# Kernel tuning notes

Measured on AMD Instinct MI355X. Metric: run time of the kernel, lower is better.

## Reference

```python
import jax, jax.numpy as jnp
import numpy as np

L, H, N = 4096, 256, 64  # seq_len, hidden_size, hippo_n
EPS = 1e-5


def setup_inputs() -> dict:
    key = jax.random.key(0)
    ks = jax.random.split(key, 8)
    x = jax.random.normal(ks[0], (L, H), jnp.float32)
    # S4D-Lin style initialization for the diagonal SSM (H independent SSMs of state size N)
    Lambda_re = -0.5 * jnp.ones((H, N), jnp.float32)
    Lambda_im = jnp.tile(jnp.pi * jnp.arange(N, dtype=jnp.float32), (H, 1))
    B_re = jnp.ones((H, N), jnp.float32)
    B_im = jnp.zeros((H, N), jnp.float32)
    C_re = jax.random.normal(ks[1], (H, N), jnp.float32) * (0.5 ** 0.5)
    C_im = jax.random.normal(ks[2], (H, N), jnp.float32) * (0.5 ** 0.5)
    D = jax.random.normal(ks[3], (H,), jnp.float32)
    log_step = jax.random.uniform(ks[4], (H,), jnp.float32,
                                  minval=jnp.log(0.001), maxval=jnp.log(0.1))
    ln_w = jnp.ones((H,), jnp.float32)
    ln_b = jnp.zeros((H,), jnp.float32)
    sc = 1.0 / jnp.sqrt(jnp.float32(H))
    W1 = jax.random.normal(ks[5], (H, H), jnp.float32) * sc
    b1 = jnp.zeros((H,), jnp.float32)
    W2 = jax.random.normal(ks[6], (H, H), jnp.float32) * sc
    b2 = jnp.zeros((H,), jnp.float32)
    return {"x": x, "Lambda_re": Lambda_re, "Lambda_im": Lambda_im,
            "B_re": B_re, "B_im": B_im, "C_re": C_re, "C_im": C_im,
            "D": D, "log_step": log_step, "ln_w": ln_w, "ln_b": ln_b,
            "W1": W1, "b1": b1, "W2": W2, "b2": b2}


def reference(x, Lambda_re, Lambda_im, B_re, B_im, C_re, C_im, D, log_step,
              ln_w, ln_b, W1, b1, W2, b2):
    skip = x
    # per-token LayerNorm over the H feature axis (eqx.nn.LayerNorm, eps=1e-5)
    mu = jnp.mean(x, axis=-1, keepdims=True)
    var = jnp.mean(jnp.square(x - mu), axis=-1, keepdims=True)
    xn = (x - mu) / jnp.sqrt(var + EPS) * ln_w + ln_b  # [L, H]

    # ZOH discretization of the diagonal SSM (the cell.ssm(L) step)
    Lam = Lambda_re + 1j * Lambda_im                     # [H, N] complex64
    dt = jnp.exp(log_step)[:, None]                      # [H, 1]
    Ab = jnp.exp(Lam * dt)                               # [H, N]
    Bb = (Ab - 1.0) / Lam * (B_re + 1j * B_im)           # [H, N]
    C = C_re + 1j * C_im                                 # [H, N]

    def step(s, u):  # s: [H, N] complex state, u: [H] input at one time step
        s = Ab * s + Bb * u[:, None]
        y = 2.0 * jnp.einsum('hn,hn->h', C, s).real + D * u
        return s, y

    s0 = jnp.zeros((H, N), jnp.complex64)
    hidden, ys = jax.lax.scan(step, s0, xn)              # ys: [L, H]

    g = jax.nn.gelu(ys)
    out = (g @ W1.T + b1) * jax.nn.sigmoid(g @ W2.T + b2)  # GLU epilogue
    return (hidden, skip + out)
```

## Files before the change

kernel.cpp:

```cpp
#include <hip/hip_runtime.h>
#include <hip/hip_bf16.h>

#define LSEQ 4096
#define HDIM 256
#define NS   64
#define PC   32
#define MC   128

typedef __attribute__((ext_vector_type(8))) short short8;
typedef __attribute__((ext_vector_type(4))) float floatx4;

__device__ __forceinline__ short b16(float x) {
    __hip_bfloat16 h = __float2bfloat16(x);
    return *(reinterpret_cast<short*>(&h));
}
__device__ __forceinline__ unsigned int pk2(float a, float b) {
    return (unsigned int)(unsigned short)b16(a) | ((unsigned int)(unsigned short)b16(b) << 16);
}
__device__ __forceinline__ void cmul(float& xr, float& xi, float yr, float yi) {
    float r = xr * yr - xi * yi;
    float i = xr * yi + xi * yr;
    xr = r; xi = i;
}

__global__ __launch_bounds__(256) void k_pre(const float* __restrict__ x,
                                             const float* __restrict__ lnw,
                                             const float* __restrict__ lnb,
                                             const float* __restrict__ W1,
                                             const float* __restrict__ W2,
                                             float* __restrict__ xnT,
                                             unsigned short* __restrict__ w1b,
                                             unsigned short* __restrict__ w2b) {
    int t = threadIdx.x;
    if (blockIdx.x >= 256) {
        int g = (blockIdx.x - 256) * 256 + t;
        float4 a = ((const float4*)W1)[g];
        float4 c = ((const float4*)W2)[g];
        ushort4 o1, o2;
        o1.x = (unsigned short)b16(a.x); o1.y = (unsigned short)b16(a.y);
        o1.z = (unsigned short)b16(a.z); o1.w = (unsigned short)b16(a.w);
        o2.x = (unsigned short)b16(c.x); o2.y = (unsigned short)b16(c.y);
        o2.z = (unsigned short)b16(c.z); o2.w = (unsigned short)b16(c.w);
        ((ushort4*)w1b)[g] = o1;
        ((ushort4*)w2b)[g] = o2;
        return;
    }
    __shared__ float tile[16][257];
    __shared__ float smu[16], srs[16];
    int l0 = blockIdx.x * 16;
#pragma unroll
    for (int i = 0; i < 16; ++i)
        tile[i][t] = x[(size_t)(l0 + i) * HDIM + t];
    __syncthreads();
    int wv = t >> 6, lane = t & 63;
#pragma unroll
    for (int k = 0; k < 4; ++k) {
        int i = wv * 4 + k;
        float s = 0.f, s2 = 0.f;
#pragma unroll
        for (int q = 0; q < 4; ++q) {
            float v = tile[i][lane + 64 * q];
            s += v; s2 += v * v;
        }
#pragma unroll
        for (int o = 32; o; o >>= 1) {
            s  += __shfl_xor(s, o);
            s2 += __shfl_xor(s2, o);
        }
        if (lane == 0) {
            float m = s * (1.0f / HDIM);
            smu[i] = m;
            srs[i] = rsqrtf(s2 * (1.0f / HDIM) - m * m + 1e-5f);
        }
    }
    __syncthreads();
    float wh = lnw[t], bh = lnb[t];
    float o[16];
#pragma unroll
    for (int i = 0; i < 16; ++i)
        o[i] = (tile[i][t] - smu[i]) * srs[i] * wh + bh;
    float4* dst = (float4*)(xnT + (size_t)t * LSEQ + l0);
#pragma unroll
    for (int k = 0; k < 4; ++k)
        dst[k] = make_float4(o[4 * k], o[4 * k + 1], o[4 * k + 2], o[4 * k + 3]);
}

__device__ __forceinline__ void ssm_consts(const float* Lre, const float* Lim,
                                           const float* Bre, const float* Bim,
                                           float dt, int idx,
                                           float& are, float& aim, float& bre, float& bim) {
    float lre = Lre[idx], lim = Lim[idx];
    float er = expf(lre * dt);
    float sa, ca;
    sincosf(lim * dt, &sa, &ca);
    are = er * ca; aim = er * sa;
    float inv = 1.0f / (lre * lre + lim * lim);
    float nre = are - 1.0f, nim = aim;
    float tre = (nre * lre + nim * lim) * inv;
    float tim = (nim * lre - nre * lim) * inv;
    float br = Bre[idx], bi = Bim[idx];
    bre = tre * br - tim * bi;
    bim = tre * bi + tim * br;
}

__global__ __launch_bounds__(256) void k_scan(const float* __restrict__ xnT,
                                              const float* __restrict__ Lre,
                                              const float* __restrict__ Lim,
                                              const float* __restrict__ Bre,
                                              const float* __restrict__ Bim,
                                              const float* __restrict__ Cre,
                                              const float* __restrict__ Cim,
                                              const float* __restrict__ Dv,
                                              const float* __restrict__ lstep,
                                              __hip_bfloat16* __restrict__ gb,
                                              float* __restrict__ hid,
                                              int interleaved) {
    __shared__ __align__(16) unsigned char ldsb[60672];
    short* ubf = (short*)(ldsb);
    short* Tm  = (short*)(ldsb + 8704);
    float* Ff  = (float*)(ldsb + 43520);
    short* S0s = (short*)(ldsb + 43520);
    float* Kt  = (float*)(ldsb + 60160);

    int h = blockIdx.x;
    int tid = threadIdx.x;
    int wv = __builtin_amdgcn_readfirstlane(tid) >> 6;
    int lane = tid & 63;
    int l15 = lane & 15, q = lane >> 4;
    const float* uh = xnT + (size_t)h * LSEQ;

    float dt = expf(lstep[h]);
    float Dh = Dv[h];

    float are, aim, bre, bim;
    ssm_consts(Lre, Lim, Bre, Bim, dt, h * NS + lane, are, aim, bre, bim);
    float cre = Cre[h * NS + lane], cim = Cim[h * NS + lane];

    float A8r = are, A8i = aim;
    cmul(A8r, A8i, A8r, A8i); cmul(A8r, A8i, A8r, A8i); cmul(A8r, A8i, A8r, A8i);
    float A16r = A8r, A16i = A8i;  cmul(A16r, A16i, A16r, A16i);
    float A32r = A16r, A32i = A16i; cmul(A32r, A32i, A32r, A32i);
    float A64r = A32r, A64i = A32i; cmul(A64r, A64i, A64r, A64i);

#pragma unroll
    for (int k = 0; k < 4; ++k) {
        int i4 = k * 1024 + tid * 4;
        float4 v = *(const float4*)(uh + i4);
        int c = i4 >> 7, col = i4 & 127;
        unsigned int* d = (unsigned int*)(ubf + c * 136 + col);
        d[0] = pk2(v.x, v.y);
        d[1] = pk2(v.z, v.w);
    }

    {
        float cbre = cre * bre - cim * bim;
        float cbim = cre * bim + cim * bre;
        float pr = 1.f, pi = 0.f;
        if (wv & 1) cmul(pr, pi, A32r, A32i);
        if (wv & 2) cmul(pr, pi, A64r, A64i);
        for (int i = 0; i < 32; ++i) {
            float kj = 2.f * (cbre * pr - cbim * pi);
#pragma unroll
            for (int o = 1; o <= 32; o <<= 1) kj += __shfl_xor(kj, o);
            if (lane == 0) Kt[32 * wv + i] = kj;
            cmul(pr, pi, are, aim);
        }
    }
    __syncthreads();

#pragma unroll 4
    for (int it = 0; it < 64; ++it) {
        int idx = it * 256 + tid;
        int row = idx >> 7, col = idx & 127;
        float kv = Kt[(row - col) & 127];
        Tm[row * 136 + col] = (col <= row) ? b16(kv) : (short)0;
    }

    {
        int n2 = 16 * wv + l15;
        float are2, aim2, bre2, bim2;
        ssm_consts(Lre, Lim, Bre, Bim, dt, h * NS + n2, are2, aim2, bre2, bim2);
        float B8r = are2, B8i = aim2;
        cmul(B8r, B8i, B8r, B8i); cmul(B8r, B8i, B8r, B8i); cmul(B8r, B8i, B8r, B8i);
        float B16r = B8r, B16i = B8i;  cmul(B16r, B16i, B16r, B16i);
        float B32r = B16r, B32i = B16i; cmul(B32r, B32i, B32r, B32i);
        float B64r = B32r, B64i = B32i; cmul(B64r, B64i, B64r, B64i);

        floatx4 fR[2], fI[2];
#pragma unroll
        for (int nt = 0; nt < 2; ++nt) { fR[nt] = (floatx4){0,0,0,0}; fI[nt] = (floatx4){0,0,0,0}; }

#pragma unroll
        for (int ks = 0; ks < 4; ++ks) {
            int m8 = 15 - 4 * ks - q;
            float sR = 1.f, sI = 0.f, tR, tI;
            tR = sR * B8r - sI * B8i;  tI = sR * B8i + sI * B8r;
            sR = (m8 & 1) ? tR : sR;   sI = (m8 & 1) ? tI : sI;
            tR = sR * B16r - sI * B16i; tI = sR * B16i + sI * B16r;
            sR = (m8 & 2) ? tR : sR;   sI = (m8 & 2) ? tI : sI;
            tR = sR * B32r - sI * B32i; tI = sR * B32i + sI * B32r;
            sR = (m8 & 4) ? tR : sR;   sI = (m8 & 4) ? tI : sI;
            tR = sR * B64r - sI * B64i; tI = sR * B64i + sI * B64r;
            sR = (m8 & 8) ? tR : sR;   sI = (m8 & 8) ? tI : sI;
            short8 aR, aI;
            float curR = sR, curI = sI;
#pragma unroll
            for (int e = 7; e >= 0; --e) {
                aR[e] = b16(bre2 * curR - bim2 * curI);
                aI[e] = b16(bre2 * curI + bim2 * curR);
                if (e) cmul(curR, curI, are2, aim2);
            }
#pragma unroll
            for (int nt = 0; nt < 2; ++nt) {
                short8 bf = *(short8*)(ubf + (16 * nt + l15) * 136 + 32 * ks + 8 * q);
                fR[nt] = __builtin_amdgcn_mfma_f32_16x16x32_bf16(aR, bf, fR[nt], 0, 0, 0);
                fI[nt] = __builtin_amdgcn_mfma_f32_16x16x32_bf16(aI, bf, fI[nt], 0, 0, 0);
            }
        }
#pragma unroll
        for (int nt = 0; nt < 2; ++nt) {
            int c = 16 * nt + l15;
            float* fp = Ff + c * 130;
#pragma unroll
            for (int reg = 0; reg < 4; ++reg) {
                int ns = 16 * wv + q * 4 + reg;
                fp[ns]      = fR[nt][reg];
                fp[65 + ns] = fI[nt][reg];
            }
        }
    }
    __syncthreads();

    if (wv == 0) {
        float a128r = A64r, a128i = A64i;
        cmul(a128r, a128i, A64r, A64i);
        float sre = 0.f, sim = 0.f;
        for (int c = 0; c < PC; ++c) {
            float fre = Ff[c * 130 + lane];
            float fim = Ff[c * 130 + 65 + lane];
            ((unsigned int*)(ldsb + 43520 + 272 * c))[lane] = pk2(sre, sim);
            float nr = fmaf(a128r, sre, fmaf(-a128i, sim, fre));
            float ni = fmaf(a128r, sim, fmaf( a128i, sre, fim));
            sre = nr; sim = ni;
        }
        if (interleaved) {
            ((float2*)hid)[h * NS + lane] = make_float2(sre, sim);
        } else {
            hid[h * NS + lane] = sre;
        }
    }

    floatx4 Y[2][2];
#pragma unroll
    for (int mi = 0; mi < 2; ++mi)
#pragma unroll
        for (int nt = 0; nt < 2; ++nt) Y[mi][nt] = (floatx4){0, 0, 0, 0};

#pragma unroll
    for (int ks = 0; ks < 4; ++ks) {
        short8 bf0 = *(short8*)(ubf + l15 * 136 + 32 * ks + 8 * q);
        short8 bf1 = *(short8*)(ubf + (16 + l15) * 136 + 32 * ks + 8 * q);
#pragma unroll
        for (int mi = 0; mi < 2; ++mi) {
            int row = 16 * (2 * wv + mi) + l15;
            short8 ta = *(short8*)(Tm + row * 136 + 32 * ks + 8 * q);
            Y[mi][0] = __builtin_amdgcn_mfma_f32_16x16x32_bf16(ta, bf0, Y[mi][0], 0, 0, 0);
            Y[mi][1] = __builtin_amdgcn_mfma_f32_16x16x32_bf16(ta, bf1, Y[mi][1], 0, 0, 0);
        }
    }
    __syncthreads();

    {
        float pr = 1.f, pi = 0.f;
        if (wv & 1) cmul(pr, pi, A32r, A32i);
        if (wv & 2) cmul(pr, pi, A64r, A64i);
        cmul(pr, pi, are, aim);
        for (int i = 0; i < 32; ++i) {
            int t = 32 * wv + i;
            float er =  2.f * (cre * pr - cim * pi);
            float en = -2.f * (cre * pi + cim * pr);
            ((unsigned int*)(ldsb + 8704 + 272 * t))[lane] = pk2(er, en);
            cmul(pr, pi, are, aim);
        }
    }
    __syncthreads();

#pragma unroll
    for (int ks = 0; ks < 4; ++ks) {
        short8 sf0 = *(short8*)(S0s + l15 * 136 + 32 * ks + 8 * q);
        short8 sf1 = *(short8*)(S0s + (16 + l15) * 136 + 32 * ks + 8 * q);
#pragma unroll
        for (int mi = 0; mi < 2; ++mi) {
            int row = 16 * (2 * wv + mi) + l15;
            short8 ea = *(short8*)(Tm + row * 136 + 32 * ks + 8 * q);
            Y[mi][0] = __builtin_amdgcn_mfma_f32_16x16x32_bf16(ea, sf0, Y[mi][0], 0, 0, 0);
            Y[mi][1] = __builtin_amdgcn_mfma_f32_16x16x32_bf16(ea, sf1, Y[mi][1], 0, 0, 0);
        }
    }

#pragma unroll
    for (int mi = 0; mi < 2; ++mi) {
#pragma unroll
        for (int nt = 0; nt < 2; ++nt) {
#pragma unroll
            for (int reg = 0; reg < 4; ++reg) {
                int t = 16 * (2 * wv + mi) + q * 4 + reg;
                int c = 16 * nt + l15;
                int l = c * MC + t;
                float u = uh[l];
                float y = Y[mi][nt][reg] + Dh * u;
                float z = 0.7978845608028654f * fmaf(0.044715f, y * y * y, y);
                float e = __expf(2.f * z);
                float th = 1.f - 2.f / (e + 1.f);
                float gg = 0.5f * y * (1.f + th);
                gb[((size_t)l << 8) + h] = __float2bfloat16(gg);
            }
        }
    }
}

__global__ __launch_bounds__(64) void k_glu_mfma(const unsigned short* __restrict__ gbs,
                                                 const unsigned short* __restrict__ w1b,
                                                 const unsigned short* __restrict__ w2b,
                                                 const float* __restrict__ b1v,
                                                 const float* __restrict__ b2v,
                                                 const float* __restrict__ x,
                                                 float* __restrict__ out) {
    int bx = blockIdx.x;
    int m0 = (bx >> 3) * 32;
    int n0 = (bx & 7) * 32;
    int lane = threadIdx.x;
    int t = lane & 15, q = lane >> 4;

    floatx4 acc[2][2][2];
#pragma unroll
    for (int a = 0; a < 2; ++a)
#pragma unroll
        for (int b = 0; b < 2; ++b)
#pragma unroll
            for (int g = 0; g < 2; ++g)
                acc[a][b][g] = (floatx4){0.f, 0.f, 0.f, 0.f};

    const unsigned short* A0  = gbs + (size_t)(m0 + t) * HDIM + q * 8;
    const unsigned short* A1  = A0 + 16 * HDIM;
    const unsigned short* B10 = w1b + (size_t)(n0 + t) * HDIM + q * 8;
    const unsigned short* B11 = B10 + 16 * HDIM;
    const unsigned short* B20 = w2b + (size_t)(n0 + t) * HDIM + q * 8;
    const unsigned short* B21 = B20 + 16 * HDIM;

#pragma unroll
    for (int ks = 0; ks < 8; ++ks) {
        int off = ks * 32;
        short8 a0  = *(const short8*)(A0  + off);
        short8 a1  = *(const short8*)(A1  + off);
        short8 b10 = *(const short8*)(B10 + off);
        short8 b11 = *(const short8*)(B11 + off);
        short8 b20 = *(const short8*)(B20 + off);
        short8 b21 = *(const short8*)(B21 + off);
        acc[0][0][0] = __builtin_amdgcn_mfma_f32_16x16x32_bf16(a0, b10, acc[0][0][0], 0, 0, 0);
        acc[0][1][0] = __builtin_amdgcn_mfma_f32_16x16x32_bf16(a0, b11, acc[0][1][0], 0, 0, 0);
        acc[1][0][0] = __builtin_amdgcn_mfma_f32_16x16x32_bf16(a1, b10, acc[1][0][0], 0, 0, 0);
        acc[1][1][0] = __builtin_amdgcn_mfma_f32_16x16x32_bf16(a1, b11, acc[1][1][0], 0, 0, 0);
        acc[0][0][1] = __builtin_amdgcn_mfma_f32_16x16x32_bf16(a0, b20, acc[0][0][1], 0, 0, 0);
        acc[0][1][1] = __builtin_amdgcn_mfma_f32_16x16x32_bf16(a0, b21, acc[0][1][1], 0, 0, 0);
        acc[1][0][1] = __builtin_amdgcn_mfma_f32_16x16x32_bf16(a1, b20, acc[1][0][1], 0, 0, 0);
        acc[1][1][1] = __builtin_amdgcn_mfma_f32_16x16x32_bf16(a1, b21, acc[1][1][1], 0, 0, 0);
    }

#pragma unroll
    for (int nt = 0; nt < 2; ++nt) {
        int hh = n0 + nt * 16 + t;
        float bb1 = b1v[hh], bb2 = b2v[hh];
#pragma unroll
        for (int mt = 0; mt < 2; ++mt) {
#pragma unroll
            for (int reg = 0; reg < 4; ++reg) {
                int l = m0 + mt * 16 + q * 4 + reg;
                float a  = acc[mt][nt][0][reg] + bb1;
                float sg = 1.f / (1.f + __expf(-(acc[mt][nt][1][reg] + bb2)));
                out[(size_t)l * HDIM + hh] = fmaf(a, sg, x[(size_t)l * HDIM + hh]);
            }
        }
    }
}

extern "C" void kernel_launch(void* const* d_in, const int* in_sizes, int n_in,
                              void* d_out, int out_size, void* d_ws, size_t ws_size,
                              hipStream_t stream) {
    (void)in_sizes; (void)n_in; (void)ws_size;
    const float* x     = (const float*)d_in[0];
    const float* Lre   = (const float*)d_in[1];
    const float* Lim   = (const float*)d_in[2];
    const float* Bre   = (const float*)d_in[3];
    const float* Bim   = (const float*)d_in[4];
    const float* Cre   = (const float*)d_in[5];
    const float* Cim   = (const float*)d_in[6];
    const float* Dv    = (const float*)d_in[7];
    const float* lstep = (const float*)d_in[8];
    const float* lnw   = (const float*)d_in[9];
    const float* lnb   = (const float*)d_in[10];
    const float* W1    = (const float*)d_in[11];
    const float* b1    = (const float*)d_in[12];
    const float* W2    = (const float*)d_in[13];
    const float* b2    = (const float*)d_in[14];

    float* ws   = (float*)d_ws;
    float* xnT  = ws;
    unsigned short* gb  = (unsigned short*)(xnT + (size_t)HDIM * LSEQ);
    unsigned short* w1b = gb + (size_t)LSEQ * HDIM;
    unsigned short* w2b = w1b + HDIM * HDIM;

    int interleaved = (out_size == LSEQ * HDIM + 2 * HDIM * NS) ? 1 : 0;
    float* hid  = (float*)d_out;
    float* outp = (float*)d_out + (interleaved ? 2 * HDIM * NS : HDIM * NS);

    k_pre      <<<256 + 64, 256, 0, stream>>>(x, lnw, lnb, W1, W2, xnT, w1b, w2b);
    k_scan     <<<HDIM, 256, 0, stream>>>(xnT, Lre, Lim, Bre, Bim, Cre, Cim,
                                          Dv, lstep, (__hip_bfloat16*)gb, hid, interleaved);
    k_glu_mfma <<<128 * 8, 64, 0, stream>>>(gb, w1b, w2b, b1, b2, x, outp);
}
```

Measured before the change: 122.9 us.

## Widen chunked SSM scan block to 16 waves with one MFMA tile per wave

Raises the k_scan block from 4 to 16 waves so each wave owns a single 16x16 output tile in the chunk GEMMs instead of four. The per-state B·A^k operand is now built once in LDS and shared, replacing the per-lane power chains recomputed inside the MFMA loop. Building the Toeplitz matrix is moved to overlap with wave 0's sequential inter-chunk state recurrence. The aim is more parallelism and latency hiding per block. In exchange it adds an extra barrier, and the larger block with its LDS use may reduce how many blocks can be resident per CU.

```diff
diff --git a/kernel.cpp b/kernel.cpp
--- a/kernel.cpp
+++ b/kernel.cpp
@@ -103,18 +103,18 @@
     bim = tre * bi + tim * br;
 }
 
-__global__ __launch_bounds__(256) void k_scan(const float* __restrict__ xnT,
-                                              const float* __restrict__ Lre,
-                                              const float* __restrict__ Lim,
-                                              const float* __restrict__ Bre,
-                                              const float* __restrict__ Bim,
-                                              const float* __restrict__ Cre,
-                                              const float* __restrict__ Cim,
-                                              const float* __restrict__ Dv,
-                                              const float* __restrict__ lstep,
-                                              __hip_bfloat16* __restrict__ gb,
-                                              float* __restrict__ hid,
-                                              int interleaved) {
+__global__ __launch_bounds__(1024) void k_scan(const float* __restrict__ xnT,
+                                               const float* __restrict__ Lre,
+                                               const float* __restrict__ Lim,
+                                               const float* __restrict__ Bre,
+                                               const float* __restrict__ Bim,
+                                               const float* __restrict__ Cre,
+                                               const float* __restrict__ Cim,
+                                               const float* __restrict__ Dv,
+                                               const float* __restrict__ lstep,
+                                               __hip_bfloat16* __restrict__ gb,
+                                               float* __restrict__ hid,
+                                               int interleaved) {
     __shared__ __align__(16) unsigned char ldsb[60672];
     short* ubf = (short*)(ldsb);
     short* Tm  = (short*)(ldsb + 8704);
@@ -127,6 +127,7 @@
     int wv = __builtin_amdgcn_readfirstlane(tid) >> 6;
     int lane = tid & 63;
     int l15 = lane & 15, q = lane >> 4;
+    int mt = wv >> 1, nt = wv & 1;
     const float* uh = xnT + (size_t)h * LSEQ;
 
     float dt = expf(lstep[h]);
@@ -136,15 +137,15 @@
     ssm_consts(Lre, Lim, Bre, Bim, dt, h * NS + lane, are, aim, bre, bim);
     float cre = Cre[h * NS + lane], cim = Cim[h * NS + lane];
 
-    float A8r = are, A8i = aim;
-    cmul(A8r, A8i, A8r, A8i); cmul(A8r, A8i, A8r, A8i); cmul(A8r, A8i, A8r, A8i);
-    float A16r = A8r, A16i = A8i;  cmul(A16r, A16i, A16r, A16i);
-    float A32r = A16r, A32i = A16i; cmul(A32r, A32i, A32r, A32i);
-    float A64r = A32r, A64i = A32i; cmul(A64r, A64i, A64r, A64i);
-
-#pragma unroll
-    for (int k = 0; k < 4; ++k) {
-        int i4 = k * 1024 + tid * 4;
+    float A2r = are, A2i = aim;   cmul(A2r, A2i, are, aim);
+    float A4r = A2r, A4i = A2i;   cmul(A4r, A4i, A2r, A2i);
+    float A8r = A4r, A8i = A4i;   cmul(A8r, A8i, A4r, A4i);
+    float A16r = A8r, A16i = A8i;  cmul(A16r, A16i, A8r, A8i);
+    float A32r = A16r, A32i = A16i; cmul(A32r, A32i, A16r, A16i);
+    float A64r = A32r, A64i = A32i; cmul(A64r, A64i, A32r, A32i);
+
+    {
+        int i4 = tid * 4;
         float4 v = *(const float4*)(uh + i4);
         int c = i4 >> 7, col = i4 & 127;
         unsigned int* d = (unsigned int*)(ubf + c * 136 + col);
@@ -156,82 +157,69 @@
         float cbre = cre * bre - cim * bim;
         float cbim = cre * bim + cim * bre;
         float pr = 1.f, pi = 0.f;
-        if (wv & 1) cmul(pr, pi, A32r, A32i);
-        if (wv & 2) cmul(pr, pi, A64r, A64i);
-        for (int i = 0; i < 32; ++i) {
+        if (wv & 1) cmul(pr, pi, A8r, A8i);
+        if (wv & 2) cmul(pr, pi, A16r, A16i);
+        if (wv & 4) cmul(pr, pi, A32r, A32i);
+        if (wv & 8) cmul(pr, pi, A64r, A64i);
+#pragma unroll
+        for (int i = 0; i < 8; ++i) {
             float kj = 2.f * (cbre * pr - cbim * pi);
 #pragma unroll
             for (int o = 1; o <= 32; o <<= 1) kj += __shfl_xor(kj, o);
-            if (lane == 0) Kt[32 * wv + i] = kj;
+            if (lane == 0) Kt[8 * wv + i] = kj;
             cmul(pr, pi, are, aim);
         }
     }
-    __syncthreads();
-
-#pragma unroll 4
-    for (int it = 0; it < 64; ++it) {
-        int idx = it * 256 + tid;
-        int row = idx >> 7, col = idx & 127;
-        float kv = Kt[(row - col) & 127];
-        Tm[row * 136 + col] = (col <= row) ? b16(kv) : (short)0;
-    }
-
-    {
-        int n2 = 16 * wv + l15;
-        float are2, aim2, bre2, bim2;
-        ssm_consts(Lre, Lim, Bre, Bim, dt, h * NS + n2, are2, aim2, bre2, bim2);
-        float B8r = are2, B8i = aim2;
-        cmul(B8r, B8i, B8r, B8i); cmul(B8r, B8i, B8r, B8i); cmul(B8r, B8i, B8r, B8i);
-        float B16r = B8r, B16i = B8i;  cmul(B16r, B16i, B16r, B16i);
-        float B32r = B16r, B32i = B16i; cmul(B32r, B32i, B32r, B32i);
-        float B64r = B32r, B64i = B32i; cmul(B64r, B64i, B64r, B64i);
-
-        floatx4 fR[2], fI[2];
-#pragma unroll
-        for (int nt = 0; nt < 2; ++nt) { fR[nt] = (floatx4){0,0,0,0}; fI[nt] = (floatx4){0,0,0,0}; }
-
+
+    {
+        int v = 15 - wv;
+        float pr = 1.f, pi = 0.f;
+        if (v & 1) cmul(pr, pi, A8r, A8i);
+        if (v & 2) cmul(pr, pi, A16r, A16i);
+        if (v & 4) cmul(pr, pi, A32r, A32i);
+        if (v & 8) cmul(pr, pi, A64r, A64i);
+        short8 rr, ri;
+#pragma unroll
+        for (int i = 0; i < 8; ++i) {
+            rr[7 - i] = b16(bre * pr - bim * pi);
+            ri[7 - i] = b16(bre * pi + bim * pr);
+            cmul(pr, pi, are, aim);
+        }
+        *(short8*)(Tm + lane * 136 + 8 * wv) = rr;
+        *(short8*)(Tm + (64 + lane) * 136 + 8 * wv) = ri;
+    }
+    __syncthreads();
+
+    {
+        floatx4 fa = (floatx4){0.f, 0.f, 0.f, 0.f};
 #pragma unroll
         for (int ks = 0; ks < 4; ++ks) {
-            int m8 = 15 - 4 * ks - q;
-            float sR = 1.f, sI = 0.f, tR, tI;
-            tR = sR * B8r - sI * B8i;  tI = sR * B8i + sI * B8r;
-            sR = (m8 & 1) ? tR : sR;   sI = (m8 & 1) ? tI : sI;
-            tR = sR * B16r - sI * B16i; tI = sR * B16i + sI * B16r;
-            sR = (m8 & 2) ? tR : sR;   sI = (m8 & 2) ? tI : sI;
-            tR = sR * B32r - sI * B32i; tI = sR * B32i + sI * B32r;
-            sR = (m8 & 4) ? tR : sR;   sI = (m8 & 4) ? tI : sI;
-            tR = sR * B64r - sI * B64i; tI = sR * B64i + sI * B64r;
-            sR = (m8 & 8) ? tR : sR;   sI = (m8 & 8) ? tI : sI;
-            short8 aR, aI;
-            float curR = sR, curI = sI;
-#pragma unroll
-            for (int e = 7; e >= 0; --e) {
-                aR[e] = b16(bre2 * curR - bim2 * curI);
-                aI[e] = b16(bre2 * curI + bim2 * curR);
-                if (e) cmul(curR, curI, are2, aim2);
+            short8 am = *(short8*)(Tm + (16 * mt + l15) * 136 + 32 * ks + 8 * q);
+            short8 bu = *(short8*)(ubf + (16 * nt + l15) * 136 + 32 * ks + 8 * q);
+            fa = __builtin_amdgcn_mfma_f32_16x16x32_bf16(am, bu, fa, 0, 0, 0);
+        }
+        int c = 16 * nt + l15;
+        float* fp = Ff + c * 130;
+        int sbase = 16 * mt + 4 * q;
+#pragma unroll
+        for (int reg = 0; reg < 4; ++reg) {
+            int s = sbase + reg;
+            fp[(mt < 4) ? s : (1 + s)] = fa[reg];
+        }
+    }
+    __syncthreads();
+
+    if (wv != 0) {
+#pragma unroll
+        for (int it = 0; it < 18; ++it) {
+            int idx = it * 960 + (tid - 64);
+            if (idx < 128 * 128) {
+                int row = idx >> 7, col = idx & 127;
+                float kv = Kt[(row - col) & 127];
+                Tm[row * 136 + col] = (col <= row) ? b16(kv) : (short)0;
             }
-#pragma unroll
-            for (int nt = 0; nt < 2; ++nt) {
-                short8 bf = *(short8*)(ubf + (16 * nt + l15) * 136 + 32 * ks + 8 * q);
-                fR[nt] = __builtin_amdgcn_mfma_f32_16x16x32_bf16(aR, bf, fR[nt], 0, 0, 0);
-                fI[nt] = __builtin_amdgcn_mfma_f32_16x16x32_bf16(aI, bf, fI[nt], 0, 0, 0);
-            }
-        }
-#pragma unroll
-        for (int nt = 0; nt < 2; ++nt) {
-            int c = 16 * nt + l15;
-            float* fp = Ff + c * 130;
-#pragma unroll
-            for (int reg = 0; reg < 4; ++reg) {
-                int ns = 16 * wv + q * 4 + reg;
-                fp[ns]      = fR[nt][reg];
-                fp[65 + ns] = fI[nt][reg];
-            }
-        }
-    }
-    __syncthreads();
-
-    if (wv == 0) {
+        }
+    } else {
         float a128r = A64r, a128i = A64i;
         cmul(a128r, a128i, A64r, A64i);
         float sre = 0.f, sim = 0.f;
@@ -249,34 +237,26 @@
             hid[h * NS + lane] = sre;
         }
     }
-
-    floatx4 Y[2][2];
-#pragma unroll
-    for (int mi = 0; mi < 2; ++mi)
-#pragma unroll
-        for (int nt = 0; nt < 2; ++nt) Y[mi][nt] = (floatx4){0, 0, 0, 0};
-
+    __syncthreads();
+
+    floatx4 Y = (floatx4){0.f, 0.f, 0.f, 0.f};
 #pragma unroll
     for (int ks = 0; ks < 4; ++ks) {
-        short8 bf0 = *(short8*)(ubf + l15 * 136 + 32 * ks + 8 * q);
-        short8 bf1 = *(short8*)(ubf + (16 + l15) * 136 + 32 * ks + 8 * q);
-#pragma unroll
-        for (int mi = 0; mi < 2; ++mi) {
-            int row = 16 * (2 * wv + mi) + l15;
-            short8 ta = *(short8*)(Tm + row * 136 + 32 * ks + 8 * q);
-            Y[mi][0] = __builtin_amdgcn_mfma_f32_16x16x32_bf16(ta, bf0, Y[mi][0], 0, 0, 0);
-            Y[mi][1] = __builtin_amdgcn_mfma_f32_16x16x32_bf16(ta, bf1, Y[mi][1], 0, 0, 0);
-        }
-    }
-    __syncthreads();
-
-    {
-        float pr = 1.f, pi = 0.f;
-        if (wv & 1) cmul(pr, pi, A32r, A32i);
-        if (wv & 2) cmul(pr, pi, A64r, A64i);
-        cmul(pr, pi, are, aim);
-        for (int i = 0; i < 32; ++i) {
-            int t = 32 * wv + i;
+        short8 ta = *(short8*)(Tm + (16 * mt + l15) * 136 + 32 * ks + 8 * q);
+        short8 bu = *(short8*)(ubf + (16 * nt + l15) * 136 + 32 * ks + 8 * q);
+        Y = __builtin_amdgcn_mfma_f32_16x16x32_bf16(ta, bu, Y, 0, 0, 0);
+    }
+    __syncthreads();
+
+    {
+        float pr = are, pi = aim;
+        if (wv & 1) cmul(pr, pi, A8r, A8i);
+        if (wv & 2) cmul(pr, pi, A16r, A16i);
+        if (wv & 4) cmul(pr, pi, A32r, A32i);
+        if (wv & 8) cmul(pr, pi, A64r, A64i);
+#pragma unroll
+        for (int i = 0; i < 8; ++i) {
+            int t = 8 * wv + i;
             float er =  2.f * (cre * pr - cim * pi);
             float en = -2.f * (cre * pi + cim * pr);
             ((unsigned int*)(ldsb + 8704 + 272 * t))[lane] = pk2(er, en);
@@ -287,34 +267,24 @@
 
 #pragma unroll
     for (int ks = 0; ks < 4; ++ks) {
-        short8 sf0 = *(short8*)(S0s + l15 * 136 + 32 * ks + 8 * q);
-        short8 sf1 = *(short8*)(S0s + (16 + l15) * 136 + 32 * ks + 8 * q);
-#pragma unroll
-        for (int mi = 0; mi < 2; ++mi) {
-            int row = 16 * (2 * wv + mi) + l15;
-            short8 ea = *(short8*)(Tm + row * 136 + 32 * ks + 8 * q);
-            Y[mi][0] = __builtin_amdgcn_mfma_f32_16x16x32_bf16(ea, sf0, Y[mi][0], 0, 0, 0);
-            Y[mi][1] = __builtin_amdgcn_mfma_f32_16x16x32_bf16(ea, sf1, Y[mi][1], 0, 0, 0);
-        }
-    }
-
-#pragma unroll
-    for (int mi = 0; mi < 2; ++mi) {
-#pragma unroll
-        for (int nt = 0; nt < 2; ++nt) {
-#pragma unroll
-            for (int reg = 0; reg < 4; ++reg) {
-                int t = 16 * (2 * wv + mi) + q * 4 + reg;
-                int c = 16 * nt + l15;
-                int l = c * MC + t;
-                float u = uh[l];
-                float y = Y[mi][nt][reg] + Dh * u;
-                float z = 0.7978845608028654f * fmaf(0.044715f, y * y * y, y);
-                float e = __expf(2.f * z);
-                float th = 1.f - 2.f / (e + 1.f);
-                float gg = 0.5f * y * (1.f + th);
-                gb[((size_t)l << 8) + h] = __float2bfloat16(gg);
-            }
+        short8 ea = *(short8*)(Tm + (16 * mt + l15) * 136 + 32 * ks + 8 * q);
+        short8 sf = *(short8*)(S0s + (16 * nt + l15) * 136 + 32 * ks + 8 * q);
+        Y = __builtin_amdgcn_mfma_f32_16x16x32_bf16(ea, sf, Y, 0, 0, 0);
+    }
+
+    {
+        int c = 16 * nt + l15;
+#pragma unroll
+        for (int reg = 0; reg < 4; ++reg) {
+            int t = 16 * mt + 4 * q + reg;
+            int l = c * MC + t;
+            float u = uh[l];
+            float y = Y[reg] + Dh * u;
+            float z = 0.7978845608028654f * fmaf(0.044715f, y * y * y, y);
+            float e = __expf(2.f * z);
+            float th = 1.f - 2.f / (e + 1.f);
+            float gg = 0.5f * y * (1.f + th);
+            gb[((size_t)l << 8) + h] = __float2bfloat16(gg);
         }
     }
 }
@@ -415,7 +385,7 @@
     float* outp = (float*)d_out + (interleaved ? 2 * HDIM * NS : HDIM * NS);
 
     k_pre      <<<256 + 64, 256, 0, stream>>>(x, lnw, lnb, W1, W2, xnT, w1b, w2b);
-    k_scan     <<<HDIM, 256, 0, stream>>>(xnT, Lre, Lim, Bre, Bim, Cre, Cim,
-                                          Dv, lstep, (__hip_bfloat16*)gb, hid, interleaved);
+    k_scan     <<<HDIM, 1024, 0, stream>>>(xnT, Lre, Lim, Bre, Bim, Cre, Cim,
+                                           Dv, lstep, (__hip_bfloat16*)gb, hid, interleaved);
     k_glu_mfma <<<128 * 8, 64, 0, stream>>>(gb, w1b, w2b, b1, b2, x, outp);
 }
```

Result: faster. 114.6 us (-6.8%).
